# Kernel tuning notes

Hardware: AMD Instinct MI355X
Metric: run time of the kernel (lower is better)

The kernel has to match this reference:

```python
import jax, jax.numpy as jnp
import numpy as np

B, L, D, H, NL = 4, 2048, 1024, 4, 2
HD = D // H
FF = 4 * D
EPS = 1e-5


def layernorm(x, g, b):
    mu = jnp.mean(x, axis=-1, keepdims=True)
    var = jnp.mean(jnp.square(x - mu), axis=-1, keepdims=True)
    return (x - mu) * jax.lax.rsqrt(var + EPS) * g + b


def setup_inputs() -> dict:
    key = jax.random.key(0)
    ks = jax.random.split(key, 8)
    std = 0.02
    return {
        "x": jax.random.normal(ks[0], (B, L, 3 * D), dtype=jnp.float32),
        "w3d": jax.random.normal(ks[1], (D, 3 * D), dtype=jnp.float32) * std,
        "b3d": jnp.zeros((D,), jnp.float32),
        "ln1_g": jnp.ones((NL, D), jnp.float32),
        "ln1_b": jnp.zeros((NL, D), jnp.float32),
        "wqkv": jax.random.normal(ks[2], (NL, 3 * D, D), dtype=jnp.float32) * std,
        "bqkv": jnp.zeros((NL, 3 * D), jnp.float32),
        "wproj": jax.random.normal(ks[3], (NL, D, D), dtype=jnp.float32) * std,
        "bproj": jnp.zeros((NL, D), jnp.float32),
        "ln2_g": jnp.ones((NL, D), jnp.float32),
        "ln2_b": jnp.zeros((NL, D), jnp.float32),
        "w1": jax.random.normal(ks[4], (NL, FF, D), dtype=jnp.float32) * std,
        "b1": jnp.zeros((NL, FF), jnp.float32),
        "w2": jax.random.normal(ks[5], (NL, D, FF), dtype=jnp.float32) * std,
        "b2": jnp.zeros((NL, D), jnp.float32),
        "lnf_g": jnp.ones((D,), jnp.float32),
        "lnf_b": jnp.zeros((D,), jnp.float32),
    }


def reference(x, w3d, b3d, ln1_g, ln1_b, wqkv, bqkv, wproj, bproj,
              ln2_g, ln2_b, w1, b1, w2, b2, lnf_g, lnf_b):
    h = jnp.einsum('bli,di->bld', x, w3d) + b3d
    scale = 1.0 / jnp.sqrt(jnp.float32(HD))
    for i in range(NL):
        # attention block
        res = h
        hn = layernorm(h, ln1_g[i], ln1_b[i])
        qkv = jnp.einsum('bld,ed->ble', hn, wqkv[i]) + bqkv[i]  # [B,L,3D]
        qkv = qkv.reshape(B, L, 3, H, HD)
        q, k, v = qkv[:, :, 0], qkv[:, :, 1], qkv[:, :, 2]  # [B,L,H,HD]
        attn = jnp.einsum('bqhd,bkhd->bhqk', q, k) * scale
        attn = jax.nn.softmax(attn, axis=-1)
        o = jnp.einsum('bhqk,bkhd->bqhd', attn, v).reshape(B, L, D)
        h = res + jnp.einsum('bld,ed->ble', o, wproj[i]) + bproj[i]
        # FFN block
        res = h
        hn = layernorm(h, ln2_g[i], ln2_b[i])
        f = jnp.einsum('bld,fd->blf', hn, w1[i]) + b1[i]
        f = jax.nn.gelu(f, approximate=False)  # torch nn.GELU default is exact
        h = res + jnp.einsum('blf,df->bld', f, w2[i]) + b2[i]
    return layernorm(h, lnf_g, lnf_b)
```

## Files before the change

### kernel.cpp

```cpp
#include <hip/hip_runtime.h>
#include <cstdint>
#include <cstddef>

#define BATCH   4
#define L_SEQ   2048
#define DMODEL  1024
#define NHEAD   4
#define HDIM    256
#define FFDIM   4096
#define MROWS   (BATCH * L_SEQ)
#define NLAYER  2

typedef __bf16 bf16_t;
typedef __bf16 bf16x8 __attribute__((ext_vector_type(8)));
typedef __bf16 bf16x4 __attribute__((ext_vector_type(4)));
typedef float  floatx4 __attribute__((ext_vector_type(4)));

__device__ __forceinline__ void async_cp16(const void* g, void* l) {
  auto gp = reinterpret_cast<__attribute__((address_space(1))) void*>(
      reinterpret_cast<uintptr_t>(g));
  auto lp = reinterpret_cast<__attribute__((address_space(3))) void*>(
      reinterpret_cast<uintptr_t>(l));
  __builtin_amdgcn_global_load_lds(gp, lp, 16, 0, 0);
}

__global__ __launch_bounds__(256)
void cvt_f32_bf16(const float* __restrict__ in, bf16_t* __restrict__ out, int n4) {
  int i = blockIdx.x * 256 + threadIdx.x;
  if (i >= n4) return;
  float4 v = ((const float4*)in)[i];
  bf16x4 ov = { (bf16_t)v.x, (bf16_t)v.y, (bf16_t)v.z, (bf16_t)v.w };
  ((bf16x4*)out)[i] = ov;
}

template<bool BF16OUT>
__global__ __launch_bounds__(256)
void ln_kernel(const float* __restrict__ x, const float* __restrict__ gw,
               const float* __restrict__ bw, void* __restrict__ outp) {
  const int row = blockIdx.x;
  const int tid = threadIdx.x;
  const float4 v = ((const float4*)(x + (size_t)row * DMODEL))[tid];
  float s  = v.x + v.y + v.z + v.w;
  float ss = v.x * v.x + v.y * v.y + v.z * v.z + v.w * v.w;
#pragma unroll
  for (int o = 32; o > 0; o >>= 1) {
    s  += __shfl_xor(s, o);
    ss += __shfl_xor(ss, o);
  }
  __shared__ float red0[4], red1[4];
  const int wv = tid >> 6;
  if ((tid & 63) == 0) { red0[wv] = s; red1[wv] = ss; }
  __syncthreads();
  s  = red0[0] + red0[1] + red0[2] + red0[3];
  ss = red1[0] + red1[1] + red1[2] + red1[3];
  const float mu  = s * (1.0f / DMODEL);
  const float var = ss * (1.0f / DMODEL) - mu * mu;
  const float rs  = rsqrtf(var + 1e-5f);
  const float4 g4 = ((const float4*)gw)[tid];
  const float4 b4 = ((const float4*)bw)[tid];
  const float o0 = (v.x - mu) * rs * g4.x + b4.x;
  const float o1 = (v.y - mu) * rs * g4.y + b4.y;
  const float o2 = (v.z - mu) * rs * g4.z + b4.z;
  const float o3 = (v.w - mu) * rs * g4.w + b4.w;
  if (BF16OUT) {
    bf16x4 ov = { (bf16_t)o0, (bf16_t)o1, (bf16_t)o2, (bf16_t)o3 };
    ((bf16x4*)outp)[(size_t)row * (DMODEL / 4) + tid] = ov;
  } else {
    float4 ov = { o0, o1, o2, o3 };
    ((float4*)outp)[(size_t)row * (DMODEL / 4) + tid] = ov;
  }
}

__global__ __launch_bounds__(512, 2)
void flash_attn(const bf16_t* __restrict__ Q, const bf16_t* __restrict__ K,
                const bf16_t* __restrict__ VT, bf16_t* __restrict__ O) {
  __shared__ bf16_t lsK[64 * 256];
  __shared__ bf16_t lsV[256 * 64];
  const int tid = threadIdx.x, wave = tid >> 6, lane = tid & 63;
  const int lane15 = lane & 15, quad = lane >> 4;
  const int z = blockIdx.y, qt = blockIdx.x;
  const bf16_t* Qz = Q + (size_t)z * L_SEQ * HDIM;
  const bf16_t* Kz = K + (size_t)z * L_SEQ * HDIM;
  const bf16_t* Vz = VT + (size_t)z * HDIM * L_SEQ;

  const int qrow = qt * 128 + wave * 16 + lane15;
  bf16x8 qf[8];
#pragma unroll
  for (int kc = 0; kc < 8; ++kc)
    qf[kc] = *(const bf16x8*)(Qz + (size_t)qrow * HDIM + kc * 32 + quad * 8);

  floatx4 oacc[16] = {};
  float m_run = -1e30f, l_run = 0.f;

  const int krl = lane >> 5, kp = lane & 31;
  const int vrl = lane >> 3, vp = lane & 7;
  bf16_t* Pw = lsK + wave * 1024;

  for (int kt = 0; kt < L_SEQ; kt += 64) {
#pragma unroll
    for (int j = 0; j < 4; ++j) {
      const int i = wave * 4 + j;
      const int r = 2 * i + krl;
      const int col = ((kp & 24) | ((kp ^ r) & 7)) * 8;
      async_cp16(Kz + (size_t)(kt + r) * HDIM + col, lsK + i * 512);
      const int rv = 8 * i + vrl;
      const int colv = ((vp ^ rv) & 7) * 8;
      async_cp16(Vz + (size_t)rv * L_SEQ + kt + colv, lsV + i * 512);
    }
    __syncthreads();

    floatx4 sacc[4] = {};
#pragma unroll
    for (int kc = 0; kc < 8; ++kc) {
#pragma unroll
      for (int mf = 0; mf < 4; ++mf) {
        const int rr = mf * 16 + lane15;
        const int c = kc * 4 + quad;
        const int phys = (c & 24) | ((c ^ rr) & 7);
        bf16x8 af = *(const bf16x8*)(lsK + rr * 256 + phys * 8);
        sacc[mf] = __builtin_amdgcn_mfma_f32_16x16x32_bf16(af, qf[kc],
                                                           sacc[mf], 0, 0, 0);
      }
    }

    float p[4][4];
    float mx = -1e30f;
#pragma unroll
    for (int mf = 0; mf < 4; ++mf)
#pragma unroll
      for (int r = 0; r < 4; ++r) {
        p[mf][r] = sacc[mf][r] * 0.0625f;
        mx = fmaxf(mx, p[mf][r]);
      }
    mx = fmaxf(mx, __shfl_xor(mx, 16));
    mx = fmaxf(mx, __shfl_xor(mx, 32));
    const float m_new = fmaxf(m_run, mx);
    const float alpha = __expf(m_run - m_new);
    float rs = 0.f;
#pragma unroll
    for (int mf = 0; mf < 4; ++mf)
#pragma unroll
      for (int r = 0; r < 4; ++r) {
        p[mf][r] = __expf(p[mf][r] - m_new);
        rs += p[mf][r];
      }
    rs += __shfl_xor(rs, 16);
    rs += __shfl_xor(rs, 32);
    l_run = l_run * alpha + rs;
    m_run = m_new;
#pragma unroll
    for (int mf = 0; mf < 16; ++mf)
#pragma unroll
      for (int r = 0; r < 4; ++r) oacc[mf][r] *= alpha;

    __syncthreads();

#pragma unroll
    for (int mf = 0; mf < 4; ++mf) {
      bf16x4 pk = { (bf16_t)p[mf][0], (bf16_t)p[mf][1],
                    (bf16_t)p[mf][2], (bf16_t)p[mf][3] };
      const int c = mf * 2 + (quad >> 1);
      const int phys = c ^ (lane15 & 7);
      *(bf16x4*)(Pw + lane15 * 64 + phys * 8 + (quad & 1) * 4) = pk;
    }

#pragma unroll
    for (int kc = 0; kc < 2; ++kc) {
      const int cb = kc * 4 + quad;
      const int pb = cb ^ (lane15 & 7);
      bf16x8 bfr = *(const bf16x8*)(Pw + lane15 * 64 + pb * 8);
#pragma unroll
      for (int mf = 0; mf < 16; ++mf) {
        const int rr = mf * 16 + lane15;
        const int phys = cb ^ (rr & 7);
        bf16x8 af = *(const bf16x8*)(lsV + rr * 64 + phys * 8);
        oacc[mf] = __builtin_amdgcn_mfma_f32_16x16x32_bf16(af, bfr,
                                                           oacc[mf], 0, 0, 0);
      }
    }
    __syncthreads();
  }

  const float inv = 1.0f / l_run;
  const int b = z >> 2, head = z & 3;
  bf16_t* orow = O + ((size_t)b * L_SEQ + qrow) * DMODEL + head * HDIM;
#pragma unroll
  for (int mf = 0; mf < 16; ++mf) {
    const int hd = mf * 16 + quad * 4;
    bf16x4 ov = { (bf16_t)(oacc[mf][0] * inv), (bf16_t)(oacc[mf][1] * inv),
                  (bf16_t)(oacc[mf][2] * inv), (bf16_t)(oacc[mf][3] * inv) };
    *(bf16x4*)(orow + hd) = ov;
  }
}

struct EpiBiasF32 {
  float* C; const float* bias; int ldc;
  __device__ __forceinline__ void store4(int, int m, int n, floatx4 v) const {
    const float bb = bias[n];
#pragma unroll
    for (int r = 0; r < 4; ++r) C[(size_t)(m + r) * ldc + n] = v[r] + bb;
  }
};
struct EpiResBiasF32 {
  float* C; const float* bias; int ldc;
  __device__ __forceinline__ void store4(int, int m, int n, floatx4 v) const {
    const float bb = bias[n];
#pragma unroll
    for (int r = 0; r < 4; ++r) {
      const size_t idx = (size_t)(m + r) * ldc + n;
      C[idx] = C[idx] + v[r] + bb;
    }
  }
};
struct EpiGeluBf16 {
  bf16_t* C; const float* bias; int ldc;
  __device__ __forceinline__ void store4(int, int m, int n, floatx4 v) const {
    const float bb = bias[n];
#pragma unroll
    for (int r = 0; r < 4; ++r) {
      const float t = v[r] + bb;
      const float g = 0.5f * t * (1.0f + erff(t * 0.7071067811865475f));
      C[(size_t)(m + r) * ldc + n] = (bf16_t)g;
    }
  }
};
struct EpiQKV {
  bf16_t *q, *k, *vT; const float* bias;
  __device__ __forceinline__ void store4(int, int m, int n, floatx4 v) const {
    const float bb = bias[n];
    const int b = m >> 11, l = m & 2047;
    const int which = n >> 10, e = n & 1023;
    const int head = e >> 8, hd = e & 255;
    const int z = b * NHEAD + head;
    if (which == 2) {
      bf16x4 ov = { (bf16_t)(v[0] + bb), (bf16_t)(v[1] + bb),
                    (bf16_t)(v[2] + bb), (bf16_t)(v[3] + bb) };
      *(bf16x4*)(vT + ((size_t)z * HDIM + hd) * L_SEQ + l) = ov;
    } else {
      bf16_t* dst = (which == 0 ? q : k) + ((size_t)z * L_SEQ + l) * HDIM + hd;
#pragma unroll
      for (int r = 0; r < 4; ++r) dst[(size_t)r * HDIM] = (bf16_t)(v[r] + bb);
    }
  }
};

template<class Epi>
__global__ __launch_bounds__(256, 3)
void gemm_bt(const bf16_t* __restrict__ A, int lda, long strideA,
             const bf16_t* __restrict__ B, int ldb, long strideB,
             int K, Epi epi) {
  __shared__ bf16_t lsA[128 * 64];
  __shared__ bf16_t lsB[128 * 64];
  const int tid  = threadIdx.x;
  const int wave = tid >> 6, lane = tid & 63;
  const int z = blockIdx.z;
  A += (size_t)z * strideA;
  B += (size_t)z * strideB;
  const int m0 = blockIdx.y * 128, n0 = blockIdx.x * 128;

  const int rl = lane >> 3, p = lane & 7;
  const int csw = (p ^ rl) * 8;
  const int rbase = wave * 32 + rl;
  const bf16_t* gA = A + (size_t)(m0 + rbase) * lda + csw;
  const bf16_t* gB = B + (size_t)(n0 + rbase) * ldb + csw;
  bf16_t* lA = &lsA[wave * 32 * 64];
  bf16_t* lB = &lsB[wave * 32 * 64];

  const int wm = wave >> 1, wn = wave & 1;
  const int lane15 = lane & 15, quad = lane >> 4;
  const int arow = wm * 64 + lane15;
  const int brow = wn * 64 + lane15;
  const int sw = lane15 & 7;
  const int koff0 = ((quad + 0) ^ sw) * 8;
  const int koff1 = ((quad + 4) ^ sw) * 8;

  floatx4 acc[4][4] = {};

  for (int k0 = 0; k0 < K; k0 += 64) {
#pragma unroll
    for (int j = 0; j < 4; ++j) {
      async_cp16(gA + k0 + (size_t)j * 8 * lda, lA + j * 8 * 64);
      async_cp16(gB + k0 + (size_t)j * 8 * ldb, lB + j * 8 * 64);
    }
    __syncthreads();
#pragma unroll
    for (int kk = 0; kk < 2; ++kk) {
      const int ko = kk ? koff1 : koff0;
      bf16x8 af[4], bfr[4];
#pragma unroll
      for (int i = 0; i < 4; ++i)
        af[i] = *(const bf16x8*)&lsA[(arow + i * 16) * 64 + ko];
#pragma unroll
      for (int j = 0; j < 4; ++j)
        bfr[j] = *(const bf16x8*)&lsB[(brow + j * 16) * 64 + ko];
#pragma unroll
      for (int i = 0; i < 4; ++i)
#pragma unroll
        for (int j = 0; j < 4; ++j)
          acc[i][j] = __builtin_amdgcn_mfma_f32_16x16x32_bf16(af[i], bfr[j],
                                                              acc[i][j], 0, 0, 0);
    }
    __syncthreads();
  }

#pragma unroll
  for (int i = 0; i < 4; ++i) {
    const int mbase = m0 + wm * 64 + i * 16 + quad * 4;
#pragma unroll
    for (int j = 0; j < 4; ++j) {
      const int nloc = n0 + wn * 64 + j * 16 + lane15;
      epi.store4(z, mbase, nloc, acc[i][j]);
    }
  }
}

extern "C" void kernel_launch(void* const* d_in, const int* in_sizes, int n_in,
                              void* d_out, int out_size, void* d_ws, size_t ws_size,
                              hipStream_t stream) {
  const float* x_in  = (const float*)d_in[0];
  const float* w3d   = (const float*)d_in[1];
  const float* b3d   = (const float*)d_in[2];
  const float* ln1g  = (const float*)d_in[3];
  const float* ln1b  = (const float*)d_in[4];
  const float* wqkv  = (const float*)d_in[5];
  const float* bqkv  = (const float*)d_in[6];
  const float* wproj = (const float*)d_in[7];
  const float* bproj = (const float*)d_in[8];
  const float* ln2g  = (const float*)d_in[9];
  const float* ln2b  = (const float*)d_in[10];
  const float* w1    = (const float*)d_in[11];
  const float* b1    = (const float*)d_in[12];
  const float* w2    = (const float*)d_in[13];
  const float* b2    = (const float*)d_in[14];
  const float* lnfg  = (const float*)d_in[15];
  const float* lnfb  = (const float*)d_in[16];
  float* out = (float*)d_out;

  char* ws = (char*)d_ws;
  size_t off = 0;
  auto alloc = [&](size_t bytes) -> void* {
    void* p = ws + off;
    off = (off + bytes + 255) & ~(size_t)255;
    return p;
  };
  float*  h      = (float*) alloc((size_t)MROWS * DMODEL * 4);
  bf16_t* hn     = (bf16_t*)alloc((size_t)MROWS * DMODEL * 2);
  bf16_t* w3db   = (bf16_t*)alloc((size_t)DMODEL * 3 * DMODEL * 2);
  bf16_t* wqkvb  = (bf16_t*)alloc((size_t)NLAYER * 3 * DMODEL * DMODEL * 2);
  bf16_t* wprojb = (bf16_t*)alloc((size_t)NLAYER * DMODEL * DMODEL * 2);
  bf16_t* w1b    = (bf16_t*)alloc((size_t)NLAYER * FFDIM * DMODEL * 2);
  bf16_t* w2b    = (bf16_t*)alloc((size_t)NLAYER * DMODEL * FFDIM * 2);
  bf16_t* xb     = (bf16_t*)alloc((size_t)MROWS * 3 * DMODEL * 2);
  bf16_t* qb     = (bf16_t*)alloc((size_t)MROWS * DMODEL * 2);
  bf16_t* kb     = (bf16_t*)alloc((size_t)MROWS * DMODEL * 2);
  bf16_t* vT     = (bf16_t*)alloc((size_t)MROWS * DMODEL * 2);
  bf16_t* ob     = (bf16_t*)alloc((size_t)MROWS * DMODEL * 2);
  bf16_t* f      = (bf16_t*)alloc((size_t)MROWS * FFDIM * 2);
  (void)ws_size; (void)in_sizes; (void)n_in; (void)out_size;

  auto cvt = [&](const float* src, bf16_t* dst, size_t n) {
    int n4 = (int)(n / 4);
    cvt_f32_bf16<<<(n4 + 255) / 256, 256, 0, stream>>>(src, dst, n4);
  };
  cvt(x_in,  xb,     (size_t)MROWS * 3 * DMODEL);
  cvt(w3d,   w3db,   (size_t)DMODEL * 3 * DMODEL);
  cvt(wqkv,  wqkvb,  (size_t)NLAYER * 3 * DMODEL * DMODEL);
  cvt(wproj, wprojb, (size_t)NLAYER * DMODEL * DMODEL);
  cvt(w1,    w1b,    (size_t)NLAYER * FFDIM * DMODEL);
  cvt(w2,    w2b,    (size_t)NLAYER * DMODEL * FFDIM);

  gemm_bt<<<dim3(DMODEL / 128, MROWS / 128, 1), 256, 0, stream>>>(
      xb, 3 * DMODEL, 0L, w3db, 3 * DMODEL, 0L, 3 * DMODEL,
      EpiBiasF32{h, b3d, DMODEL});

  for (int i = 0; i < NLAYER; ++i) {
    ln_kernel<true><<<MROWS, 256, 0, stream>>>(h, ln1g + i * DMODEL,
                                               ln1b + i * DMODEL, hn);
    gemm_bt<<<dim3(3 * DMODEL / 128, MROWS / 128, 1), 256, 0, stream>>>(
        hn, DMODEL, 0L, wqkvb + (size_t)i * 3 * DMODEL * DMODEL, DMODEL, 0L,
        DMODEL, EpiQKV{qb, kb, vT, bqkv + i * 3 * DMODEL});
    flash_attn<<<dim3(L_SEQ / 128, BATCH * NHEAD), 512, 0, stream>>>(
        qb, kb, vT, ob);
    gemm_bt<<<dim3(DMODEL / 128, MROWS / 128, 1), 256, 0, stream>>>(
        ob, DMODEL, 0L, wprojb + (size_t)i * DMODEL * DMODEL, DMODEL, 0L,
        DMODEL, EpiResBiasF32{h, bproj + i * DMODEL, DMODEL});
    ln_kernel<true><<<MROWS, 256, 0, stream>>>(h, ln2g + i * DMODEL,
                                               ln2b + i * DMODEL, hn);
    gemm_bt<<<dim3(FFDIM / 128, MROWS / 128, 1), 256, 0, stream>>>(
        hn, DMODEL, 0L, w1b + (size_t)i * FFDIM * DMODEL, DMODEL, 0L, DMODEL,
        EpiGeluBf16{f, b1 + i * FFDIM, FFDIM});
    gemm_bt<<<dim3(DMODEL / 128, MROWS / 128, 1), 256, 0, stream>>>(
        f, FFDIM, 0L, w2b + (size_t)i * DMODEL * FFDIM, FFDIM, 0L, FFDIM,
        EpiResBiasF32{h, b2 + i * DMODEL, DMODEL});
  }

  ln_kernel<false><<<MROWS, 256, 0, stream>>>(h, lnfg, lnfb, out);
}
```

Before: 1.272 ms.

## Add 256x256 pipelined GEMM, XCD-aware block remap, smaller flash-attn tiles

Adds a new 256x256-tile GEMM kernel with 512 threads, double-buffered LDS, async global-to-LDS staging interleaved with MFMA quarters, and s_setprio around the MFMA groups. It is used for the QKV and FFN-up projections. Block IDs in the GEMMs and flash attention are remapped so that consecutive blocks land on the same XCD, which is meant to improve L2 reuse. Flash attention moves to 64-query tiles with 256 threads per block, giving more blocks for better occupancy at the cost of more K/V reloads.

```diff
diff --git a/kernel.cpp b/kernel.cpp
--- a/kernel.cpp
+++ b/kernel.cpp
@@ -71,19 +71,21 @@
   }
 }
 
-__global__ __launch_bounds__(512, 2)
+__global__ __launch_bounds__(256, 2)
 void flash_attn(const bf16_t* __restrict__ Q, const bf16_t* __restrict__ K,
                 const bf16_t* __restrict__ VT, bf16_t* __restrict__ O) {
   __shared__ bf16_t lsK[64 * 256];
   __shared__ bf16_t lsV[256 * 64];
   const int tid = threadIdx.x, wave = tid >> 6, lane = tid & 63;
   const int lane15 = lane & 15, quad = lane >> 4;
-  const int z = blockIdx.y, qt = blockIdx.x;
+  const int bid = blockIdx.y * 32 + blockIdx.x;
+  const int wg  = (bid & 7) * 64 + (bid >> 3);
+  const int z = wg >> 5, qt = wg & 31;
   const bf16_t* Qz = Q + (size_t)z * L_SEQ * HDIM;
   const bf16_t* Kz = K + (size_t)z * L_SEQ * HDIM;
   const bf16_t* Vz = VT + (size_t)z * HDIM * L_SEQ;
 
-  const int qrow = qt * 128 + wave * 16 + lane15;
+  const int qrow = qt * 64 + wave * 16 + lane15;
   bf16x8 qf[8];
 #pragma unroll
   for (int kc = 0; kc < 8; ++kc)
@@ -98,8 +100,8 @@
 
   for (int kt = 0; kt < L_SEQ; kt += 64) {
 #pragma unroll
-    for (int j = 0; j < 4; ++j) {
-      const int i = wave * 4 + j;
+    for (int j = 0; j < 8; ++j) {
+      const int i = wave * 8 + j;
       const int r = 2 * i + krl;
       const int col = ((kp & 24) | ((kp ^ r) & 7)) * 8;
       async_cp16(Kz + (size_t)(kt + r) * HDIM + col, lsK + i * 512);
@@ -256,7 +258,11 @@
   const int z = blockIdx.z;
   A += (size_t)z * strideA;
   B += (size_t)z * strideB;
-  const int m0 = blockIdx.y * 128, n0 = blockIdx.x * 128;
+  const int gdx = gridDim.x;
+  const int nwg = gdx * gridDim.y;
+  const int bid = blockIdx.y * gdx + blockIdx.x;
+  const int wg  = (bid & 7) * (nwg >> 3) + (bid >> 3);
+  const int m0 = (wg / gdx) * 128, n0 = (wg % gdx) * 128;
 
   const int rl = lane >> 3, p = lane & 7;
   const int csw = (p ^ rl) * 8;
@@ -306,6 +312,133 @@
 #pragma unroll
   for (int i = 0; i < 4; ++i) {
     const int mbase = m0 + wm * 64 + i * 16 + quad * 4;
+#pragma unroll
+    for (int j = 0; j < 4; ++j) {
+      const int nloc = n0 + wn * 64 + j * 16 + lane15;
+      epi.store4(z, mbase, nloc, acc[i][j]);
+    }
+  }
+}
+
+#define GVM(n)  asm volatile("s_waitcnt vmcnt(" #n ")" ::: "memory")
+#define GBARM() asm volatile("s_barrier" ::: "memory")
+
+#define READ_A(h)                                                         \
+  _Pragma("unroll") for (int i = 0; i < 4; ++i) {                         \
+    const int row = wm * 128 + ((h) * 4 + i) * 16 + lane15;               \
+    af[i][0] = *(const bf16x8*)&lsA[b][row * 64 + ko0];                   \
+    af[i][1] = *(const bf16x8*)&lsA[b][row * 64 + ko1];                   \
+  }
+#define READ_B(jp, dst)                                                   \
+  _Pragma("unroll") for (int j = 0; j < 2; ++j) {                         \
+    const int row = wn * 64 + (jp) * 32 + j * 16 + lane15;                \
+    dst[j][0] = *(const bf16x8*)&lsB[b][row * 64 + ko0];                  \
+    dst[j][1] = *(const bf16x8*)&lsB[b][row * 64 + ko1];                  \
+  }
+#define MFMA_Q(h, jp, BF)                                                 \
+  __builtin_amdgcn_s_setprio(1);                                          \
+  _Pragma("unroll") for (int kk = 0; kk < 2; ++kk)                        \
+  _Pragma("unroll") for (int i = 0; i < 4; ++i)                           \
+  _Pragma("unroll") for (int j = 0; j < 2; ++j)                           \
+    acc[(h) * 4 + i][(jp) * 2 + j] = __builtin_amdgcn_mfma_f32_16x16x32_bf16( \
+        af[i][kk], BF[j][kk], acc[(h) * 4 + i][(jp) * 2 + j], 0, 0, 0);   \
+  __builtin_amdgcn_s_setprio(0);
+
+template<class Epi>
+__global__ __launch_bounds__(512, 2)
+void gemm_bt_256(const bf16_t* __restrict__ A, int lda, long strideA,
+                 const bf16_t* __restrict__ B, int ldb, long strideB,
+                 int K, Epi epi) {
+  __shared__ bf16_t lsA[2][256 * 64];
+  __shared__ bf16_t lsB[2][256 * 64];
+  const int tid  = threadIdx.x;
+  const int wave = tid >> 6, lane = tid & 63;
+  const int z = blockIdx.z;
+  A += (size_t)z * strideA;
+  B += (size_t)z * strideB;
+  const int gdx = gridDim.x;
+  const int nwg = gdx * gridDim.y;
+  const int bid = blockIdx.y * gdx + blockIdx.x;
+  const int wg  = (bid & 7) * (nwg >> 3) + (bid >> 3);
+  const int m0 = (wg / gdx) * 256, n0 = (wg % gdx) * 256;
+
+  const int wm = wave >> 2, wn = wave & 3;
+  const int lane15 = lane & 15, quad = lane >> 4;
+  const int sw  = lane15 & 7;
+  const int ko0 = ((quad + 0) ^ sw) * 8;
+  const int ko1 = ((quad + 4) ^ sw) * 8;
+
+  const int srl  = lane >> 3;
+  const int scol = ((lane & 7) ^ (srl & 7)) * 8;
+
+  auto stageA = [&](int dst, int h, int kt) {
+#pragma unroll
+    for (int u = 0; u < 2; ++u) {
+      const int idx   = wave + u * 8;
+      const int grow0 = (h + 2 * (idx >> 3)) * 64 + (idx & 7) * 8;
+      async_cp16(A + (size_t)(m0 + grow0 + srl) * lda + kt * 64 + scol,
+                 &lsA[dst][grow0 * 64]);
+    }
+  };
+  auto stageB = [&](int dst, int h, int kt) {
+#pragma unroll
+    for (int u = 0; u < 2; ++u) {
+      const int idx   = wave + u * 8;
+      const int grow0 = h * 32 + (idx >> 2) * 64 + (idx & 3) * 8;
+      async_cp16(B + (size_t)(n0 + grow0 + srl) * ldb + kt * 64 + scol,
+                 &lsB[dst][grow0 * 64]);
+    }
+  };
+
+  floatx4 acc[8][4] = {};
+  bf16x8 af[4][2], bf0[2][2], bf1[2][2];
+
+  const int NT = K / 64;
+  stageA(0, 0, 0); stageB(0, 0, 0); stageB(0, 1, 0); stageA(0, 1, 0);
+
+  for (int t = 0; t < NT - 1; ++t) {
+    const int b = t & 1, d = b ^ 1;
+
+    GVM(4); GBARM();
+    READ_A(0); READ_B(0, bf0);
+    stageA(d, 0, t + 1);
+    MFMA_Q(0, 0, bf0);
+
+    GVM(4); GBARM();
+    READ_B(1, bf1);
+    stageB(d, 0, t + 1);
+    MFMA_Q(0, 1, bf1);
+
+    GVM(4); GBARM();
+    READ_A(1);
+    stageB(d, 1, t + 1);
+    MFMA_Q(1, 1, bf1);
+
+    GVM(4); GBARM();
+    stageA(d, 1, t + 1);
+    MFMA_Q(1, 0, bf0);
+  }
+
+  {
+    const int b = (NT - 1) & 1;
+    GVM(4); GBARM();
+    READ_A(0); READ_B(0, bf0);
+    MFMA_Q(0, 0, bf0);
+
+    GVM(2); GBARM();
+    READ_B(1, bf1);
+    MFMA_Q(0, 1, bf1);
+
+    GVM(0); GBARM();
+    READ_A(1);
+    MFMA_Q(1, 1, bf1);
+
+    MFMA_Q(1, 0, bf0);
+  }
+
+#pragma unroll
+  for (int i = 0; i < 8; ++i) {
+    const int mbase = m0 + wm * 128 + i * 16 + quad * 4;
 #pragma unroll
     for (int j = 0; j < 4; ++j) {
       const int nloc = n0 + wn * 64 + j * 16 + lane15;
@@ -376,17 +509,17 @@
   for (int i = 0; i < NLAYER; ++i) {
     ln_kernel<true><<<MROWS, 256, 0, stream>>>(h, ln1g + i * DMODEL,
                                                ln1b + i * DMODEL, hn);
-    gemm_bt<<<dim3(3 * DMODEL / 128, MROWS / 128, 1), 256, 0, stream>>>(
+    gemm_bt_256<<<dim3(3 * DMODEL / 256, MROWS / 256, 1), 512, 0, stream>>>(
         hn, DMODEL, 0L, wqkvb + (size_t)i * 3 * DMODEL * DMODEL, DMODEL, 0L,
         DMODEL, EpiQKV{qb, kb, vT, bqkv + i * 3 * DMODEL});
-    flash_attn<<<dim3(L_SEQ / 128, BATCH * NHEAD), 512, 0, stream>>>(
+    flash_attn<<<dim3(L_SEQ / 64, BATCH * NHEAD), 256, 0, stream>>>(
         qb, kb, vT, ob);
     gemm_bt<<<dim3(DMODEL / 128, MROWS / 128, 1), 256, 0, stream>>>(
         ob, DMODEL, 0L, wprojb + (size_t)i * DMODEL * DMODEL, DMODEL, 0L,
         DMODEL, EpiResBiasF32{h, bproj + i * DMODEL, DMODEL});
     ln_kernel<true><<<MROWS, 256, 0, stream>>>(h, ln2g + i * DMODEL,
                                                ln2b + i * DMODEL, hn);
-    gemm_bt<<<dim3(FFDIM / 128, MROWS / 128, 1), 256, 0, stream>>>(
+    gemm_bt_256<<<dim3(FFDIM / 256, MROWS / 256, 1), 512, 0, stream>>>(
         hn, DMODEL, 0L, w1b + (size_t)i * FFDIM * DMODEL, DMODEL, 0L, DMODEL,
         EpiGeluBf16{f, b1 + i * FFDIM, FFDIM});
     gemm_bt<<<dim3(DMODEL / 128, MROWS / 128, 1), 256, 0, stream>>>(
```

Measured after the change: 1.215 ms. 1.05x faster.
